# Performance work log

Hardware: AMD Instinct MI355X
Metric: run time of the kernel (lower is better)

## Reference

```python
import jax, jax.numpy as jnp
import numpy as np

EPS = 1e-5


def setup_inputs() -> dict:
    key = jax.random.key(0)
    ks = jax.random.split(key, 12)
    B, C, H, W = 1, 512, 64, 64
    d = C // 8
    inp = {
        "x": jax.random.normal(ks[0], (B, C, H, W), jnp.float32),
        "y": jax.random.normal(ks[1], (B, C, H, W), jnp.float32),
        "s_m": jax.random.uniform(ks[2], (H, W), jnp.float32),
        "q_m": jax.random.uniform(ks[3], (H, W), jnp.float32),
        "Wq": jax.random.normal(ks[4], (d, C), jnp.float32) * (1.0 / np.sqrt(C)),
        "bq": jnp.zeros((d,), jnp.float32),
        "Wk": jax.random.normal(ks[5], (d, C), jnp.float32) * (1.0 / np.sqrt(C)),
        "bk": jnp.zeros((d,), jnp.float32),
        "Wv": jax.random.normal(ks[6], (C, C), jnp.float32) * (1.0 / np.sqrt(C)),
        "bv": jnp.zeros((C,), jnp.float32),
        "W1": jax.random.normal(ks[7], (C, C), jnp.float32) * (1.0 / np.sqrt(C)),
        "b1": jnp.zeros((C,), jnp.float32),
        "W2": jax.random.normal(ks[8], (C, C), jnp.float32) * (1.0 / np.sqrt(C)),
        "b2": jnp.zeros((C,), jnp.float32),
        "gamma": jnp.ones((1, C, H, W), jnp.float32),
        "beta": jnp.zeros((1, C, H, W), jnp.float32),
    }
    return inp


def _conv1x1(x, Wt, b):
    # 1x1 Conv2d == per-pixel channel matmul
    return jnp.einsum("bchw,oc->bohw", x, Wt) + b[None, :, None, None]


def reference(x, y, s_m, q_m, Wq, bq, Wk, bk, Wv, bv, W1, b1, W2, b2, gamma, beta):
    B, C, H, W = x.shape
    N = H * W
    scale = (C // 8) ** (-0.5)

    q_m = jnp.where(q_m > 0.8, 1.0, 0.0).astype(x.dtype)
    x_fg = x * s_m[None, None]
    y_fg = y * q_m[None, None]

    def branch(q_in, k_in, v_in, use_max):
        q = _conv1x1(q_in, Wq, bq).reshape(B, -1, N).transpose(0, 2, 1) * scale  # [B,N,d]
        k = _conv1x1(k_in, Wk, bk).reshape(B, -1, N)                             # [B,d,N]
        v = _conv1x1(v_in, Wv, bv).reshape(B, -1, N)                             # [B,C,N]
        attn = jnp.einsum("bqd,bdk->bqk", q, k)                                  # [B,N,N]
        stat = jnp.max(attn) if use_max else jnp.min(attn)
        thr = (stat + jnp.mean(attn)) * 0.5
        attn = jnp.where(attn < thr, jnp.asarray(-999.0, attn.dtype), attn)
        attn = jax.nn.softmax(attn, axis=-1)
        out = jnp.einsum("bck,bqk->bcq", v, attn).reshape(B, C, H, W)
        h = out.transpose(0, 2, 3, 1)                                            # [B,H,W,C]
        h = jnp.maximum(h @ W1.T + b1, 0.0) @ W2.T + b2
        out = h.transpose(0, 3, 1, 2)
        # LayerNorm over all trailing dims [1,C,H,W] (B==1)
        mu = jnp.mean(out)
        var = jnp.mean((out - mu) ** 2)
        out = (out - mu) * jax.lax.rsqrt(var + EPS) * gamma + beta
        return out

    outx = branch(x_fg, y_fg, y_fg, True)
    outx = outx * s_m[None, None] + x * (1.0 - s_m)[None, None]
    outy = branch(y_fg, x, x, False)
    outy = outy * q_m[None, None] + y * (1.0 - q_m)[None, None]
    return outx, outy
```

## Files before the change

### kernel.cpp

```cpp
#include <hip/hip_runtime.h>
#include <math.h>

#define C_DIM 512
#define N_DIM 4096
#define CN (C_DIM * N_DIM)
#define SZO (N_DIM * C_DIM)
#define NN ((size_t)N_DIM * N_DIM)
#define NN_TOT ((long long)N_DIM * N_DIM)

typedef __attribute__((ext_vector_type(4))) float f32x4;
typedef __attribute__((ext_vector_type(8))) short short8;

__device__ __forceinline__ ushort f2bf(float f) {
    unsigned u = __float_as_uint(f);
    unsigned r = u + 0x7FFFu + ((u >> 16) & 1u);
    return (ushort)(r >> 16);
}
__device__ __forceinline__ float bf2f(ushort h) {
    return __uint_as_float((unsigned)h << 16);
}

__device__ __forceinline__ void gload16(const void* g, void* l) {
    __builtin_amdgcn_global_load_lds(
        (const __attribute__((address_space(1))) void*)g,
        (__attribute__((address_space(3))) void*)l, 16, 0, 0);
}

__global__ __launch_bounds__(256) void setup_all(
    const float* __restrict__ x, const float* __restrict__ y,
    ushort* __restrict__ xbT, ushort* __restrict__ ybT,
    const float* __restrict__ Wv, const float* __restrict__ W1,
    const float* __restrict__ W2, ushort* __restrict__ Wvb,
    ushort* __restrict__ W1b, ushort* __restrict__ W2b,
    const float* __restrict__ Wq, const float* __restrict__ Wk,
    float* __restrict__ PX)
{
    __shared__ float t[64][65];
    __shared__ float Asw[16][130];
    __shared__ float Bsx[16][65];
    const int id = blockIdx.x;
    const int tid = threadIdx.x;

    if (id < 1024) {
        const int bx = id & 63, by = (id >> 6) & 7, bz = id >> 9;
        const float* X = bz ? y : x;
        ushort* XT = bz ? ybT : xbT;
        const int c0 = bx * 64, r0 = by * 64;
        const int ty = tid >> 4, tx = tid & 15;
        #pragma unroll
        for (int i = 0; i < 4; ++i) {
            int r = ty + i * 16;
            float4 v = *(const float4*)&X[(size_t)(r0 + r) * N_DIM + c0 + tx * 4];
            t[r][tx * 4 + 0] = v.x; t[r][tx * 4 + 1] = v.y;
            t[r][tx * 4 + 2] = v.z; t[r][tx * 4 + 3] = v.w;
        }
        __syncthreads();
        #pragma unroll
        for (int i = 0; i < 4; ++i) {
            int nn = ty + i * 16;
            ushort4 o;
            o.x = f2bf(t[tx * 4 + 0][nn]); o.y = f2bf(t[tx * 4 + 1][nn]);
            o.z = f2bf(t[tx * 4 + 2][nn]); o.w = f2bf(t[tx * 4 + 3][nn]);
            *(ushort4*)&XT[(size_t)(c0 + nn) * C_DIM + r0 + tx * 4] = o;
        }
        return;
    }
    if (id < 1792) {
        const int i2 = id - 1024;
        const int bx = i2 & 255, by = i2 >> 8;
        const float* in  = (by == 0) ? Wv : (by == 1) ? W1 : W2;
        ushort*      out = (by == 0) ? Wvb : (by == 1) ? W1b : W2b;
        int i = (bx * 256 + tid) * 4;
        float4 v = *(const float4*)&in[i];
        ushort4 o = { f2bf(v.x), f2bf(v.y), f2bf(v.z), f2bf(v.w) };
        *(ushort4*)&out[i] = o;
        return;
    }
    {
        const int i3 = id - 1792;
        const int ntile = i3 & 63;
        const int srcT  = (i3 >> 6) & 1;
        const int kz    = i3 >> 7;
        const float* X = srcT ? y : x;
        const int n0 = ntile * 64;
        const int ty = tid >> 4, tx = tid & 15;
        float accQ[4][4] = {}, accK[4][4] = {};
        const int kbase = kz * 256;

        for (int k0 = kbase; k0 < kbase + 256; k0 += 16) {
            #pragma unroll
            for (int i = 0; i < 2; ++i) {
                int wi = tid + i * 256;
                int mm = wi >> 2;
                int kq = (wi & 3) * 4;
                const float* Wp = (mm < 64) ? &Wq[(size_t)mm * 512]
                                            : &Wk[(size_t)(mm - 64) * 512];
                float4 w4 = *(const float4*)&Wp[k0 + kq];
                Asw[kq + 0][mm] = w4.x; Asw[kq + 1][mm] = w4.y;
                Asw[kq + 2][mm] = w4.z; Asw[kq + 3][mm] = w4.w;
            }
            {
                int kk = tid >> 4, nq = (tid & 15) * 4;
                *(float4*)&Bsx[kk][nq] = *(const float4*)&X[(size_t)(k0 + kk) * N_DIM + n0 + nq];
            }
            __syncthreads();
            #pragma unroll
            for (int kk = 0; kk < 16; ++kk) {
                float aq[4], ak[4], b[4];
                #pragma unroll
                for (int r = 0; r < 4; ++r) { aq[r] = Asw[kk][ty * 4 + r]; ak[r] = Asw[kk][64 + ty * 4 + r]; }
                #pragma unroll
                for (int c = 0; c < 4; ++c) b[c] = Bsx[kk][tx * 4 + c];
                #pragma unroll
                for (int r = 0; r < 4; ++r)
                    #pragma unroll
                    for (int c = 0; c < 4; ++c) {
                        accQ[r][c] = fmaf(aq[r], b[c], accQ[r][c]);
                        accK[r][c] = fmaf(ak[r], b[c], accK[r][c]);
                    }
            }
            __syncthreads();
        }
        float* dst = PX + ((size_t)(kz * 2 + srcT) * 128) * N_DIM;
        #pragma unroll
        for (int r = 0; r < 4; ++r) {
            float4 oq = make_float4(accQ[r][0], accQ[r][1], accQ[r][2], accQ[r][3]);
            *(float4*)&dst[(size_t)(ty * 4 + r) * N_DIM + n0 + tx * 4] = oq;
            float4 ok = make_float4(accK[r][0], accK[r][1], accK[r][2], accK[r][3]);
            *(float4*)&dst[(size_t)(64 + ty * 4 + r) * N_DIM + n0 + tx * 4] = ok;
        }
    }
}

__global__ __launch_bounds__(256) void qkfinish(
    const float* __restrict__ PX,
    const float* __restrict__ s_m, const float* __restrict__ q_m,
    const float* __restrict__ bq, const float* __restrict__ bk,
    ushort* __restrict__ QF0, ushort* __restrict__ KF0,
    ushort* __restrict__ QF1, ushort* __restrict__ KF1)
{
    int gid = blockIdx.x * 256 + threadIdx.x;
    int lane = gid & 63;
    int rest = gid >> 6;
    int blk = rest & 255;
    int tensor = rest >> 8;
    int fr = lane & 15, quad = lane >> 4;
    int n = blk * 16 + fr;

    int srcT, rowbase, isQ;
    const float* bias;
    ushort* dst;
    float mv, scale;
    if (tensor == 0)      { srcT = 0; rowbase = 0;  isQ = 1; bias = bq; dst = QF0; scale = 0.125f; mv = s_m[n]; }
    else if (tensor == 1) { srcT = 1; rowbase = 64; isQ = 0; bias = bk; dst = KF0; scale = 1.0f;   mv = (q_m[n] > 0.8f) ? 1.0f : 0.0f; }
    else if (tensor == 2) { srcT = 1; rowbase = 0;  isQ = 1; bias = bq; dst = QF1; scale = 0.125f; mv = (q_m[n] > 0.8f) ? 1.0f : 0.0f; }
    else                  { srcT = 0; rowbase = 64; isQ = 0; bias = bk; dst = KF1; scale = 1.0f;   mv = 1.0f; }

    ushort hi0[8], lo0[8], hi1[8], lo1[8];
    #pragma unroll
    for (int j = 0; j < 8; ++j) {
        int d0 = quad * 8 + j, d1 = 32 + d0;
        float v0 = 0.0f, v1 = 0.0f;
        #pragma unroll
        for (int kz = 0; kz < 2; ++kz) {
            size_t base = ((size_t)(kz * 2 + srcT) * 128 + rowbase);
            v0 += PX[(base + d0) * N_DIM + n];
            v1 += PX[(base + d1) * N_DIM + n];
        }
        v0 = (v0 * mv + bias[d0]) * scale;
        v1 = (v1 * mv + bias[d1]) * scale;
        hi0[j] = f2bf(v0); lo0[j] = f2bf(v0 - bf2f(hi0[j]));
        hi1[j] = f2bf(v1); lo1[j] = f2bf(v1 - bf2f(hi1[j]));
    }
    auto wr8 = [&](int kstep, const ushort* v) {
        size_t base = ((size_t)(blk * 6 + kstep) * 64 + lane) * 8;
        *(ushort4*)&dst[base]     = *(const ushort4*)&v[0];
        *(ushort4*)&dst[base + 4] = *(const ushort4*)&v[4];
    };
    wr8(0, hi0); wr8(1, hi1);
    if (isQ) { wr8(2, hi0); wr8(3, hi1); wr8(4, lo0); wr8(5, lo1); }
    else     { wr8(2, lo0); wr8(3, lo1); wr8(4, hi0); wr8(5, hi1); }
}

__device__ __forceinline__ void scores_mfma(
    const ushort* __restrict__ QF, const ushort* __restrict__ KF,
    int m0, int n0, int wr, int wc, int lane, f32x4 acc[4][4])
{
    const int blkA0 = (m0 + wr) >> 4;
    const int blkB0 = (n0 + wc) >> 4;
    #pragma unroll
    for (int s = 0; s < 6; ++s) {
        short8 af[4], bf[4];
        #pragma unroll
        for (int mr = 0; mr < 4; ++mr)
            af[mr] = *(const short8*)&QF[((size_t)((blkA0 + mr) * 6 + s) * 64 + lane) * 8];
        #pragma unroll
        for (int nc = 0; nc < 4; ++nc)
            bf[nc] = *(const short8*)&KF[((size_t)((blkB0 + nc) * 6 + s) * 64 + lane) * 8];
        #pragma unroll
        for (int mr = 0; mr < 4; ++mr)
            #pragma unroll
            for (int nc = 0; nc < 4; ++nc)
                acc[mr][nc] = __builtin_amdgcn_mfma_f32_16x16x32_bf16(
                    af[mr], bf[nc], acc[mr][nc], 0, 0, 0);
    }
}

__global__ __launch_bounds__(256) void vproj_p1(
    const ushort* __restrict__ Wvb,
    const ushort* __restrict__ xbT, const ushort* __restrict__ ybT,
    const float* __restrict__ bv, const float* __restrict__ q_m,
    ushort* __restrict__ Vb,
    const ushort* __restrict__ QF0, const ushort* __restrict__ KF0,
    const ushort* __restrict__ QF1, const ushort* __restrict__ KF1,
    float* __restrict__ part, float* __restrict__ rowmaxp)
{
    __shared__ ushort As[2][128 * 32];
    __shared__ ushort Bs[2][128 * 32];
    __shared__ float wrm[2][128];
    __shared__ float red[256];
    const int id = blockIdx.x;
    const int tid = threadIdx.x;
    const int lane = tid & 63;
    const int wid  = tid >> 6;

    if (id < 256) {
        const int bxn = id & 31;
        const int bym = (id >> 5) & 3;
        const int br  = id >> 7;
        const ushort* A = Wvb;
        const ushort* B = br ? xbT : ybT;
        const int m0 = bym * 128, n0 = bxn * 128;
        const int wr = (wid >> 1) * 64, wc = (wid & 1) * 64;
        const int lrow = lane >> 2;
        const int kbl  = lane & 3;
        const int K = 512;

        auto stage = [&](int buf, int t) {
            #pragma unroll
            for (int c = wid; c < 16; c += 4) {
                if (c < 8) {
                    int r = c * 16 + lrow;
                    int kb = kbl ^ ((r >> 1) & 3);
                    gload16(A + (size_t)(m0 + r) * K + t * 32 + kb * 8, &As[buf][c * 512]);
                } else {
                    int cb = c - 8;
                    int r = cb * 16 + lrow;
                    int kb = kbl ^ ((r >> 1) & 3);
                    gload16(B + (size_t)(n0 + r) * K + t * 32 + kb * 8, &Bs[buf][cb * 512]);
                }
            }
        };

        f32x4 acc[4][4] = {};
        const int fr = lane & 15;
        const int kq = lane >> 4;
        stage(0, 0);
        asm volatile("s_waitcnt vmcnt(0)" ::: "memory");
        __syncthreads();
        int cur = 0;
        for (int t = 0; t < 16; ++t) {
            if (t + 1 < 16) stage(cur ^ 1, t + 1);
            short8 af[4], bf[4];
            #pragma unroll
            for (int mr = 0; mr < 4; ++mr) {
                int rA = wr + mr * 16 + fr;
                af[mr] = *(const short8*)&As[cur][rA * 32 + (kq ^ ((rA >> 1) & 3)) * 8];
            }
            #pragma unroll
            for (int nc = 0; nc < 4; ++nc) {
                int rB = wc + nc * 16 + fr;
                bf[nc] = *(const short8*)&Bs[cur][rB * 32 + (kq ^ ((rB >> 1) & 3)) * 8];
            }
            #pragma unroll
            for (int mr = 0; mr < 4; ++mr)
                #pragma unroll
                for (int nc = 0; nc < 4; ++nc)
                    acc[mr][nc] = __builtin_amdgcn_mfma_f32_16x16x32_bf16(
                        af[mr], bf[nc], acc[mr][nc], 0, 0, 0);
            asm volatile("s_waitcnt vmcnt(0)" ::: "memory");
            __syncthreads();
            cur ^= 1;
        }
        const int orow = (lane >> 4) * 4;
        const int ocol = lane & 15;
        float mcol[4];
        #pragma unroll
        for (int nc = 0; nc < 4; ++nc) {
            int gn = n0 + wc + nc * 16 + ocol;
            mcol[nc] = br ? 1.0f : ((q_m[gn] > 0.8f) ? 1.0f : 0.0f);
        }
        ushort* Obf = Vb + (size_t)br * CN;
        #pragma unroll
        for (int mr = 0; mr < 4; ++mr)
            #pragma unroll
            for (int j = 0; j < 4; ++j) {
                int gm = m0 + wr + mr * 16 + orow + j;
                float brow = bv[gm];
                #pragma unroll
                for (int nc = 0; nc < 4; ++nc) {
                    int gn = n0 + wc + nc * 16 + ocol;
                    float v = acc[mr][nc][j] * mcol[nc] + brow;
                    Obf[(size_t)gm * N_DIM + gn] = f2bf(v);
                }
            }
        return;
    }

    {
        const int p = id - 256;
        const int bxn = p & 31;
        const int bym = (p >> 5) & 31;
        const int br  = p >> 10;
        const ushort* QF = br ? QF1 : QF0;
        const ushort* KF = br ? KF1 : KF0;
        float* pt = part + (size_t)br * 3072;
        float* rmp = rowmaxp + (size_t)br * 131072;

        const int m0 = bym * 128, n0 = bxn * 128;
        const int wr = (wid >> 1) * 64, wc = (wid & 1) * 64;
        f32x4 acc[4][4] = {};
        scores_mfma(QF, KF, m0, n0, wr, wc, lane, acc);

        float lmax = -3.4e38f, lmin = 3.4e38f, lsum = 0.0f;
        float rmx[4][4];
        #pragma unroll
        for (int mr = 0; mr < 4; ++mr)
            #pragma unroll
            for (int j = 0; j < 4; ++j) rmx[mr][j] = -3.4e38f;
        #pragma unroll
        for (int mr = 0; mr < 4; ++mr)
            #pragma unroll
            for (int nc = 0; nc < 4; ++nc)
                #pragma unroll
                for (int j = 0; j < 4; ++j) {
                    float v = acc[mr][nc][j];
                    lsum += v; lmax = fmaxf(lmax, v); lmin = fminf(lmin, v);
                    rmx[mr][j] = fmaxf(rmx[mr][j], v);
                }
        #pragma unroll
        for (int m = 1; m < 16; m <<= 1)
            #pragma unroll
            for (int mr = 0; mr < 4; ++mr)
                #pragma unroll
                for (int j = 0; j < 4; ++j)
                    rmx[mr][j] = fmaxf(rmx[mr][j], __shfl_xor(rmx[mr][j], m, 64));

        const int orow = (lane >> 4) * 4;
        if ((lane & 15) == 0) {
            #pragma unroll
            for (int mr = 0; mr < 4; ++mr)
                #pragma unroll
                for (int j = 0; j < 4; ++j)
                    wrm[wid & 1][wr + mr * 16 + orow + j] = rmx[mr][j];
        }
        __syncthreads();
        if (tid < 128) {
            float v = fmaxf(wrm[0][tid], wrm[1][tid]);
            rmp[(size_t)bxn * 4096 + m0 + tid] = v;
        }

        const int bid = bym * 32 + bxn;
        __syncthreads();
        red[tid] = lmax; __syncthreads();
        for (int s = 128; s > 0; s >>= 1) { if (tid < s) red[tid] = fmaxf(red[tid], red[tid + s]); __syncthreads(); }
        if (tid == 0) pt[bid] = red[0];
        __syncthreads();
        red[tid] = lmin; __syncthreads();
        for (int s = 128; s > 0; s >>= 1) { if (tid < s) red[tid] = fminf(red[tid], red[tid + s]); __syncthreads(); }
        if (tid == 0) pt[1024 + bid] = red[0];
        __syncthreads();
        red[tid] = lsum; __syncthreads();
        for (int s = 128; s > 0; s >>= 1) { if (tid < s) red[tid] += red[tid + s]; __syncthreads(); }
        if (tid == 0) pt[2048 + bid] = red[0];
    }
}

__global__ __launch_bounds__(256) void stats_fin2(
    const float* __restrict__ part, float* __restrict__ stats)
{
    const int br = blockIdx.x;
    part += (size_t)br * 3072;
    __shared__ float rmax[256], rmin[256];
    __shared__ double rsum[256];
    int tid = threadIdx.x;
    float m1 = -3.4e38f, m2 = 3.4e38f; double s = 0.0;
    for (int i = tid; i < 1024; i += 256) {
        m1 = fmaxf(m1, part[i]);
        m2 = fminf(m2, part[1024 + i]);
        s += (double)part[2048 + i];
    }
    rmax[tid] = m1; rmin[tid] = m2; rsum[tid] = s;
    __syncthreads();
    for (int st = 128; st > 0; st >>= 1) {
        if (tid < st) {
            rmax[tid] = fmaxf(rmax[tid], rmax[tid + st]);
            rmin[tid] = fminf(rmin[tid], rmin[tid + st]);
            rsum[tid] += rsum[tid + st];
        }
        __syncthreads();
    }
    if (tid == 0) {
        float stat = (br == 0) ? rmax[0] : rmin[0];
        float mean = (float)(rsum[0] / (double)NN_TOT);
        stats[br] = 0.5f * (stat + mean);
    }
}

__global__ __launch_bounds__(256) void scores_pass2(
    const ushort* __restrict__ QF0, const ushort* __restrict__ KF0,
    const ushort* __restrict__ QF1, const ushort* __restrict__ KF1,
    const float* __restrict__ stats, const float* __restrict__ rowmaxp,
    ushort* __restrict__ Pe, float* __restrict__ rowsump)
{
    const int br = blockIdx.z;
    const ushort* QF = br ? QF1 : QF0;
    const ushort* KF = br ? KF1 : KF0;
    ushort* P = Pe + (size_t)br * NN;
    rowsump += (size_t)br * 131072;
    rowmaxp += (size_t)br * 131072;

    const int tid = threadIdx.x;
    const int lane = tid & 63, wid = tid >> 6;
    const int m0 = blockIdx.y * 128, n0 = blockIdx.x * 128;
    const int wr = (wid >> 1) * 64, wc = (wid & 1) * 64;
    const float thr = stats[br];

    __shared__ float rowmL[128];
    if (tid < 128) {
        int r = m0 + tid;
        float m = -3.4e38f;
        #pragma unroll 8
        for (int b = 0; b < 32; ++b)
            m = fmaxf(m, rowmaxp[(size_t)b * 4096 + r]);
        rowmL[tid] = (m >= thr) ? m : -1e30f;
    }
    __syncthreads();

    f32x4 acc[4][4] = {};
    scores_mfma(QF, KF, m0, n0, wr, wc, lane, acc);

    const int orow = (lane >> 4) * 4;
    const int ocol = lane & 15;
    float rm[4][4], rs[4][4];
    #pragma unroll
    for (int mr = 0; mr < 4; ++mr)
        #pragma unroll
        for (int j = 0; j < 4; ++j) {
            rm[mr][j] = rowmL[wr + mr * 16 + orow + j];
            rs[mr][j] = 0.0f;
        }
    #pragma unroll
    for (int mr = 0; mr < 4; ++mr)
        #pragma unroll
        for (int nc = 0; nc < 4; ++nc)
            #pragma unroll
            for (int j = 0; j < 4; ++j) {
                float s = acc[mr][nc][j];
                float m = rm[mr][j];
                float e = (s < thr) ? 0.0f : __expf(s - m);
                if (m < -1e29f) e = 1.0f;
                ushort h = f2bf(e);
                rs[mr][j] += bf2f(h);
                P[(size_t)(m0 + wr + mr * 16 + orow + j) * N_DIM
                  + n0 + wc + nc * 16 + ocol] = h;
            }
    #pragma unroll
    for (int m = 1; m < 16; m <<= 1)
        #pragma unroll
        for (int mr = 0; mr < 4; ++mr)
            #pragma unroll
            for (int j = 0; j < 4; ++j)
                rs[mr][j] += __shfl_xor(rs[mr][j], m, 64);

    __shared__ float wrs[2][128];
    if ((lane & 15) == 0) {
        #pragma unroll
        for (int mr = 0; mr < 4; ++mr)
            #pragma unroll
            for (int j = 0; j < 4; ++j)
                wrs[wid & 1][wr + mr * 16 + orow + j] = rs[mr][j];
    }
    __syncthreads();
    if (tid < 128)
        rowsump[(size_t)blockIdx.x * 4096 + m0 + tid] =
            wrs[0][tid] + wrs[1][tid];
}

template<int BM, int BN>
__global__ __launch_bounds__(256) void mfma_g(
    const ushort* __restrict__ A0, const ushort* __restrict__ A1,
    const ushort* __restrict__ B0, const ushort* __restrict__ B1,
    void* __restrict__ Out, size_t outBrStride,
    int M, int N, int K, int kLen, int nkz, int swapxy,
    const float* __restrict__ bias, int biasMode,
    const float* __restrict__ mask0, int mm0,
    const float* __restrict__ mask1, int mm1,
    int doRelu, int outBf16, float* __restrict__ lnp)
{
    constexpr int WAVES_M = BM / 64;
    constexpr int WAVES_N = 4 / WAVES_M;
    constexpr int WN = BN / WAVES_N;
    constexpr int FM = 4;
    constexpr int FN = WN / 16;
    constexpr int NCHUNK = (BM + BN) / 16;

    __shared__ ushort As[2][BM * 32];
    __shared__ ushort Bs[2][BN * 32];
    const int tid  = threadIdx.x;
    const int lane = tid & 63;
    const int wid  = tid >> 6;
    const int z  = blockIdx.z;
    const int br = z / nkz;
    const int kz = z % nkz;
    const ushort* A = br ? A1 : A0;
    const ushort* B = br ? B1 : B0;
    const float* mask = br ? mask1 : mask0;
    const int maskMode = br ? mm1 : mm0;

    const int bxm = swapxy ? blockIdx.x : blockIdx.y;
    const int bxn = swapxy ? blockIdx.y : blockIdx.x;
    const int m0 = bxm * BM, n0 = bxn * BN;
    const int wm = wid / WAVES_N, wn = wid % WAVES_N;
    const int wr = wm * 64, wc = wn * WN;
    const int kOff = kz * kLen;
    const int lrow = lane >> 2;
    const int kbl  = lane & 3;

    auto stage = [&](int buf, int t) {
        #pragma unroll
        for (int c = wid; c < NCHUNK; c += 4) {
            if (c < BM / 16) {
                int r = c * 16 + lrow;
                int kb = kbl ^ ((r >> 1) & 3);
                gload16(A + (size_t)(m0 + r) * K + kOff + t * 32 + kb * 8,
                        &As[buf][c * 512]);
            } else {
                int cb = c - BM / 16;
                int r = cb * 16 + lrow;
                int kb = kbl ^ ((r >> 1) & 3);
                gload16(B + (size_t)(n0 + r) * K + kOff + t * 32 + kb * 8,
                        &Bs[buf][cb * 512]);
            }
        }
    };

    f32x4 acc[FM][FN] = {};
    const int fr = lane & 15;
    const int kq = lane >> 4;
    const int nt = kLen / 32;

    stage(0, 0);
    asm volatile("s_waitcnt vmcnt(0)" ::: "memory");
    __syncthreads();
    int cur = 0;
    for (int t = 0; t < nt; ++t) {
        if (t + 1 < nt) stage(cur ^ 1, t + 1);
        short8 af[FM], bf[FN];
        #pragma unroll
        for (int mr = 0; mr < FM; ++mr) {
            int rA = wr + mr * 16 + fr;
            af[mr] = *(const short8*)&As[cur][rA * 32 + (kq ^ ((rA >> 1) & 3)) * 8];
        }
        #pragma unroll
        for (int nc = 0; nc < FN; ++nc) {
            int rB = wc + nc * 16 + fr;
            bf[nc] = *(const short8*)&Bs[cur][rB * 32 + (kq ^ ((rB >> 1) & 3)) * 8];
        }
        #pragma unroll
        for (int mr = 0; mr < FM; ++mr)
            #pragma unroll
            for (int nc = 0; nc < FN; ++nc)
                acc[mr][nc] = __builtin_amdgcn_mfma_f32_16x16x32_bf16(
                    af[mr], bf[nc], acc[mr][nc], 0, 0, 0);
        asm volatile("s_waitcnt vmcnt(0)" ::: "memory");
        __syncthreads();
        cur ^= 1;
    }

    const int orow = (lane >> 4) * 4;
    const int ocol = lane & 15;

    if (nkz > 1) {
        float* Of = (float*)Out + (size_t)z * M * N;
        #pragma unroll
        for (int mr = 0; mr < FM; ++mr)
            #pragma unroll
            for (int nc = 0; nc < FN; ++nc)
                #pragma unroll
                for (int j = 0; j < 4; ++j) {
                    int gm = m0 + wr + mr * 16 + orow + j;
                    int gn = n0 + wc + nc * 16 + ocol;
                    Of[(size_t)gm * N + gn] = acc[mr][nc][j];
                }
        return;
    }

    float mcol[FN], bcol[FN];
    #pragma unroll
    for (int nc = 0; nc < FN; ++nc) {
        int gn = n0 + wc + nc * 16 + ocol;
        mcol[nc] = (maskMode == 0) ? 1.0f
                 : (maskMode == 1) ? mask[gn]
                                   : (mask[gn] > 0.8f ? 1.0f : 0.0f);
        bcol[nc] = (biasMode == 2) ? bias[gn] : 0.0f;
    }
    ushort* Obf = (ushort*)Out + (size_t)br * outBrStride;
    float*  Of  = (float*)Out + (size_t)br * outBrStride;
    float lsum = 0.0f, lsq = 0.0f;
    #pragma unroll
    for (int mr = 0; mr < FM; ++mr) {
        #pragma unroll
        for (int j = 0; j < 4; ++j) {
            int gm = m0 + wr + mr * 16 + orow + j;
            float brow = (biasMode == 1) ? bias[gm] : 0.0f;
            #pragma unroll
            for (int nc = 0; nc < FN; ++nc) {
                int gn = n0 + wc + nc * 16 + ocol;
                float v = acc[mr][nc][j] * mcol[nc] + brow + bcol[nc];
                if (doRelu) v = fmaxf(v, 0.0f);
                if (outBf16) Obf[(size_t)gm * N + gn] = f2bf(v);
                else         Of[(size_t)gm * N + gn] = v;
                lsum += v; lsq = fmaf(v, v, lsq);
            }
        }
    }
    if (lnp) {
        __shared__ float redS[256], redQ[256];
        redS[tid] = lsum; redQ[tid] = lsq;
        __syncthreads();
        for (int s = 128; s > 0; s >>= 1) {
            if (tid < s) { redS[tid] += redS[tid + s]; redQ[tid] += redQ[tid + s]; }
            __syncthreads();
        }
        if (tid == 0) {
            int fb = blockIdx.y * gridDim.x + blockIdx.x;
            lnp[br * 512 + fb] = redS[0];
            lnp[br * 512 + 256 + fb] = redQ[0];
        }
    }
}

__global__ __launch_bounds__(256) void reduce2row(
    const float* __restrict__ P4, const float* __restrict__ rowsump,
    ushort* __restrict__ O)
{
    const int br = blockIdx.y;
    const int tid = threadIdx.x;
    const int r0 = blockIdx.x * 2;
    __shared__ float invL[2];
    if (tid < 64) {
        int rw = tid >> 5, b = tid & 31;
        float s = rowsump[(size_t)br * 131072 + (size_t)b * 4096 + r0 + rw];
        #pragma unroll
        for (int m = 1; m < 32; m <<= 1) s += __shfl_xor(s, m, 64);
        if (b == 0) invL[rw] = 1.0f / s;
    }
    __syncthreads();
    int i = (blockIdx.x * 256 + tid) * 4;
    float sc = invL[(i >> 9) & 1];
    float4 a = *(const float4*)&P4[(size_t)(br * 2 + 0) * SZO + i];
    float4 b = *(const float4*)&P4[(size_t)(br * 2 + 1) * SZO + i];
    ushort4 o;
    o.x = f2bf((a.x + b.x) * sc);
    o.y = f2bf((a.y + b.y) * sc);
    o.z = f2bf((a.z + b.z) * sc);
    o.w = f2bf((a.w + b.w) * sc);
    *(ushort4*)&O[(size_t)br * SZO + i] = o;
}

__global__ __launch_bounds__(256) void gate_write(
    const float* __restrict__ H2, const float* __restrict__ lnp,
    const float* __restrict__ gamma, const float* __restrict__ beta,
    const float* __restrict__ x, const float* __restrict__ y,
    const float* __restrict__ s_m, const float* __restrict__ q_m,
    float* __restrict__ out)
{
    const int br = blockIdx.y;
    const int tid = threadIdx.x;
    __shared__ double rs[256], rq[256];
    rs[tid] = (double)lnp[(size_t)br * 512 + tid];
    rq[tid] = (double)lnp[(size_t)br * 512 + 256 + tid];
    __syncthreads();
    for (int st = 128; st > 0; st >>= 1) {
        if (tid < st) { rs[tid] += rs[tid + st]; rq[tid] += rq[tid + st]; }
        __syncthreads();
    }
    double muD = rs[0] / (double)CN;
    double varD = rq[0] / (double)CN - muD * muD;
    float mu = (float)muD;
    float rstd = (float)(1.0 / sqrt(varD + 1e-5));

    size_t i = ((size_t)blockIdx.x * 256 + tid) * 4;
    int n = (int)(i & (N_DIM - 1));
    float4 h = *(const float4*)&H2[(size_t)br * CN + i];
    float4 g = *(const float4*)&gamma[i];
    float4 b = *(const float4*)&beta[i];
    const float* resid = br ? y : x;
    float4 r = *(const float4*)&resid[i];
    float vals[4] = { h.x, h.y, h.z, h.w };
    float gs[4] = { g.x, g.y, g.z, g.w };
    float bs[4] = { b.x, b.y, b.z, b.w };
    float rsv[4] = { r.x, r.y, r.z, r.w };
    float os[4];
    #pragma unroll
    for (int j = 0; j < 4; ++j) {
        float mv = br ? ((q_m[n + j] > 0.8f) ? 1.0f : 0.0f) : s_m[n + j];
        float normed = (vals[j] - mu) * rstd * gs[j] + bs[j];
        os[j] = normed * mv + rsv[j] * (1.0f - mv);
    }
    float4 o; o.x = os[0]; o.y = os[1]; o.z = os[2]; o.w = os[3];
    *(float4*)&out[(size_t)br * CN + i] = o;
}

extern "C" void kernel_launch(void* const* d_in, const int* in_sizes, int n_in,
                              void* d_out, int out_size, void* d_ws, size_t ws_size,
                              hipStream_t stream)
{
    const float* x     = (const float*)d_in[0];
    const float* y     = (const float*)d_in[1];
    const float* s_m   = (const float*)d_in[2];
    const float* q_m   = (const float*)d_in[3];
    const float* Wq    = (const float*)d_in[4];
    const float* bq    = (const float*)d_in[5];
    const float* Wk    = (const float*)d_in[6];
    const float* bk    = (const float*)d_in[7];
    const float* Wv    = (const float*)d_in[8];
    const float* bv    = (const float*)d_in[9];
    const float* W1    = (const float*)d_in[10];
    const float* b1    = (const float*)d_in[11];
    const float* W2    = (const float*)d_in[12];
    const float* b2    = (const float*)d_in[13];
    const float* gamma = (const float*)d_in[14];
    const float* beta  = (const float*)d_in[15];
    float* out = (float*)d_out;

    float* ws = (float*)d_ws;
    float*  R1    = ws;
    float*  PX    = R1;
    float*  P4    = R1;
    ushort* QF0   = (ushort*)(R1 + 4194304);
    ushort* KF0   = QF0 + 786432;
    ushort* QF1   = KF0 + 786432;
    ushort* KF1   = QF1 + 786432;
    float*  SMALL = R1 + 8388608;
    float*  PART  = SMALL;
    float*  RMAXP = PART + 6144;
    float*  RSUMP = RMAXP + 262144;
    float*  LNP   = RSUMP + 262144;
    float*  STATS = LNP + 1024;
    ushort* Wvb   = (ushort*)(STATS + 64);
    ushort* W1b   = Wvb + 262144;
    ushort* W2b   = W1b + 262144;
    ushort* Vb    = W2b + 262144;
    ushort* R2    = Vb + 4194304;
    ushort* xbT   = R2;
    ushort* ybT   = R2 + 2097152;
    ushort* Pe    = R2;
    ushort* O1T   = R2;
    ushort* H1T   = R2 + 4194304;
    float*  H2    = (float*)(R2 + 8388608);

    setup_all<<<2048, 256, 0, stream>>>(
        x, y, xbT, ybT, Wv, W1, W2, Wvb, W1b, W2b, Wq, Wk, PX);

    qkfinish<<<256, 256, 0, stream>>>(PX, s_m, q_m, bq, bk, QF0, KF0, QF1, KF1);

    vproj_p1<<<2304, 256, 0, stream>>>(
        Wvb, xbT, ybT, bv, q_m, Vb, QF0, KF0, QF1, KF1, PART, RMAXP);

    stats_fin2<<<2, 256, 0, stream>>>(PART, STATS);

    scores_pass2<<<dim3(32, 32, 2), 256, 0, stream>>>(
        QF0, KF0, QF1, KF1, STATS, RMAXP, Pe, RSUMP);

    mfma_g<128, 128><<<dim3(32, 4, 4), 256, 0, stream>>>(
        Pe, Pe + NN, Vb, Vb + CN, P4, 0,
        4096, 512, 4096, 2048, 2, 1, nullptr, 0, nullptr, 0, nullptr, 0, 0, 0, nullptr);

    reduce2row<<<dim3(2048, 2), 256, 0, stream>>>(P4, RSUMP, O1T);

    mfma_g<128, 64><<<dim3(32, 8, 2), 256, 0, stream>>>(
        O1T, O1T + SZO, W1b, W1b, H1T, (size_t)SZO,
        4096, 512, 512, 512, 1, 1, b1, 2, nullptr, 0, nullptr, 0, 1, 1, nullptr);

    mfma_g<64, 128><<<dim3(32, 8, 2), 256, 0, stream>>>(
        W2b, W2b, H1T, H1T + SZO, H2, (size_t)CN,
        512, 4096, 512, 512, 1, 0, b2, 1, nullptr, 0, nullptr, 0, 0, 0, LNP);

    gate_write<<<dim3(2048, 2), 256, 0, stream>>>(
        H2, LNP, gamma, beta, x, y, s_m, q_m, out);
}
```

Before: 258.4 us.

## Move Q/K projection to split-bf16 MFMA GEMM kernel

```diff
diff --git a/kernel.cpp b/kernel.cpp
--- a/kernel.cpp
+++ b/kernel.cpp
@@ -26,25 +26,25 @@
         (__attribute__((address_space(3))) void*)l, 16, 0, 0);
 }
 
-__global__ __launch_bounds__(256) void setup_all(
+__global__ __launch_bounds__(256) void setup2(
     const float* __restrict__ x, const float* __restrict__ y,
-    ushort* __restrict__ xbT, ushort* __restrict__ ybT,
+    ushort* __restrict__ xbT, ushort* __restrict__ xlT,
+    ushort* __restrict__ ybT, ushort* __restrict__ ylT,
     const float* __restrict__ Wv, const float* __restrict__ W1,
     const float* __restrict__ W2, ushort* __restrict__ Wvb,
     ushort* __restrict__ W1b, ushort* __restrict__ W2b,
     const float* __restrict__ Wq, const float* __restrict__ Wk,
-    float* __restrict__ PX)
+    ushort* __restrict__ WqkH, ushort* __restrict__ WqkL)
 {
     __shared__ float t[64][65];
-    __shared__ float Asw[16][130];
-    __shared__ float Bsx[16][65];
     const int id = blockIdx.x;
     const int tid = threadIdx.x;
 
     if (id < 1024) {
         const int bx = id & 63, by = (id >> 6) & 7, bz = id >> 9;
         const float* X = bz ? y : x;
-        ushort* XT = bz ? ybT : xbT;
+        ushort* XH = bz ? ybT : xbT;
+        ushort* XL = bz ? ylT : xlT;
         const int c0 = bx * 64, r0 = by * 64;
         const int ty = tid >> 4, tx = tid & 15;
         #pragma unroll
@@ -58,10 +58,15 @@
         #pragma unroll
         for (int i = 0; i < 4; ++i) {
             int nn = ty + i * 16;
-            ushort4 o;
-            o.x = f2bf(t[tx * 4 + 0][nn]); o.y = f2bf(t[tx * 4 + 1][nn]);
-            o.z = f2bf(t[tx * 4 + 2][nn]); o.w = f2bf(t[tx * 4 + 3][nn]);
-            *(ushort4*)&XT[(size_t)(c0 + nn) * C_DIM + r0 + tx * 4] = o;
+            ushort4 h, l;
+            float v0 = t[tx * 4 + 0][nn], v1 = t[tx * 4 + 1][nn];
+            float v2 = t[tx * 4 + 2][nn], v3 = t[tx * 4 + 3][nn];
+            h.x = f2bf(v0); h.y = f2bf(v1); h.z = f2bf(v2); h.w = f2bf(v3);
+            l.x = f2bf(v0 - bf2f(h.x)); l.y = f2bf(v1 - bf2f(h.y));
+            l.z = f2bf(v2 - bf2f(h.z)); l.w = f2bf(v3 - bf2f(h.w));
+            size_t off = (size_t)(c0 + nn) * C_DIM + r0 + tx * 4;
+            *(ushort4*)&XH[off] = h;
+            *(ushort4*)&XL[off] = l;
         }
         return;
     }
@@ -77,59 +82,106 @@
         return;
     }
     {
-        const int i3 = id - 1792;
-        const int ntile = i3 & 63;
-        const int srcT  = (i3 >> 6) & 1;
-        const int kz    = i3 >> 7;
-        const float* X = srcT ? y : x;
-        const int n0 = ntile * 64;
-        const int ty = tid >> 4, tx = tid & 15;
-        float accQ[4][4] = {}, accK[4][4] = {};
-        const int kbase = kz * 256;
-
-        for (int k0 = kbase; k0 < kbase + 256; k0 += 16) {
-            #pragma unroll
-            for (int i = 0; i < 2; ++i) {
-                int wi = tid + i * 256;
-                int mm = wi >> 2;
-                int kq = (wi & 3) * 4;
-                const float* Wp = (mm < 64) ? &Wq[(size_t)mm * 512]
-                                            : &Wk[(size_t)(mm - 64) * 512];
-                float4 w4 = *(const float4*)&Wp[k0 + kq];
-                Asw[kq + 0][mm] = w4.x; Asw[kq + 1][mm] = w4.y;
-                Asw[kq + 2][mm] = w4.z; Asw[kq + 3][mm] = w4.w;
+        const int bx = id - 1792;
+        int i = (bx * 256 + tid) * 4;
+        int row = i >> 9;
+        const float* src = (row < 64) ? &Wq[(size_t)row * 512]
+                                      : &Wk[(size_t)(row - 64) * 512];
+        float4 v = *(const float4*)&src[i & 511];
+        ushort4 h, l;
+        h.x = f2bf(v.x); h.y = f2bf(v.y); h.z = f2bf(v.z); h.w = f2bf(v.w);
+        l.x = f2bf(v.x - bf2f(h.x)); l.y = f2bf(v.y - bf2f(h.y));
+        l.z = f2bf(v.z - bf2f(h.z)); l.w = f2bf(v.w - bf2f(h.w));
+        *(ushort4*)&WqkH[i] = h;
+        *(ushort4*)&WqkL[i] = l;
+    }
+}
+
+__global__ __launch_bounds__(256) void qkproj(
+    const ushort* __restrict__ WqkH, const ushort* __restrict__ WqkL,
+    const ushort* __restrict__ xbT, const ushort* __restrict__ xlT,
+    const ushort* __restrict__ ybT, const ushort* __restrict__ ylT,
+    float* __restrict__ PX)
+{
+    __shared__ ushort As[2][128 * 32];
+    __shared__ ushort Bs[2][128 * 32];
+    const int tid = threadIdx.x;
+    const int lane = tid & 63;
+    const int wid  = tid >> 6;
+    const int n0  = blockIdx.x * 128;
+    const int kz  = blockIdx.y;
+    const int src = blockIdx.z;
+    const ushort* XH = src ? ybT : xbT;
+    const ushort* XL = src ? ylT : xlT;
+    const int wr = (wid >> 1) * 64, wc = (wid & 1) * 64;
+    const int lrow = lane >> 2;
+    const int kbl  = lane & 3;
+
+    auto stage = [&](int buf, int tt) {
+        const ushort* Asrc = (tt >= 32) ? WqkL : WqkH;
+        const ushort* Bsrc = (tt >= 16 && tt < 32) ? XL : XH;
+        const int ko = (tt & 15) * 32;
+        #pragma unroll
+        for (int c = wid; c < 16; c += 4) {
+            if (c < 8) {
+                int r = c * 16 + lrow;
+                int kb = kbl ^ ((r >> 1) & 3);
+                gload16(Asrc + (size_t)r * 512 + ko + kb * 8, &As[buf][c * 512]);
+            } else {
+                int cb = c - 8;
+                int r = cb * 16 + lrow;
+                int kb = kbl ^ ((r >> 1) & 3);
+                gload16(Bsrc + (size_t)(n0 + r) * 512 + ko + kb * 8, &Bs[buf][cb * 512]);
             }
-            {
-                int kk = tid >> 4, nq = (tid & 15) * 4;
-                *(float4*)&Bsx[kk][nq] = *(const float4*)&X[(size_t)(k0 + kk) * N_DIM + n0 + nq];
+        }
+    };
+
+    f32x4 acc[4][4] = {};
+    const int fr = lane & 15;
+    const int kq = lane >> 4;
+    const int t0 = kz * 12;
+
+    stage(0, t0);
+    asm volatile("s_waitcnt vmcnt(0)" ::: "memory");
+    __syncthreads();
+    int cur = 0;
+    for (int s = 0; s < 12; ++s) {
+        if (s + 1 < 12) stage(cur ^ 1, t0 + s + 1);
+        short8 af[4], bf[4];
+        #pragma unroll
+        for (int mr = 0; mr < 4; ++mr) {
+            int rA = wr + mr * 16 + fr;
+            af[mr] = *(const short8*)&As[cur][rA * 32 + (kq ^ ((rA >> 1) & 3)) * 8];
+        }
+        #pragma unroll
+        for (int nc = 0; nc < 4; ++nc) {
+            int rB = wc + nc * 16 + fr;
+            bf[nc] = *(const short8*)&Bs[cur][rB * 32 + (kq ^ ((rB >> 1) & 3)) * 8];
+        }
+        #pragma unroll
+        for (int mr = 0; mr < 4; ++mr)
+            #pragma unroll
+            for (int nc = 0; nc < 4; ++nc)
+                acc[mr][nc] = __builtin_amdgcn_mfma_f32_16x16x32_bf16(
+                    af[mr], bf[nc], acc[mr][nc], 0, 0, 0);
+        asm volatile("s_waitcnt vmcnt(0)" ::: "memory");
+        __syncthreads();
+        cur ^= 1;
+    }
+
+    const int orow = (lane >> 4) * 4;
+    const int ocol = lane & 15;
+    float* Of = PX + ((size_t)(kz * 2 + src) * 128) * N_DIM;
+    #pragma unroll
+    for (int mr = 0; mr < 4; ++mr)
+        #pragma unroll
+        for (int nc = 0; nc < 4; ++nc)
+            #pragma unroll
+            for (int j = 0; j < 4; ++j) {
+                int gm = wr + mr * 16 + orow + j;
+                int gn = n0 + wc + nc * 16 + ocol;
+                Of[(size_t)gm * N_DIM + gn] = acc[mr][nc][j];
             }
-            __syncthreads();
-            #pragma unroll
-            for (int kk = 0; kk < 16; ++kk) {
-                float aq[4], ak[4], b[4];
-                #pragma unroll
-                for (int r = 0; r < 4; ++r) { aq[r] = Asw[kk][ty * 4 + r]; ak[r] = Asw[kk][64 + ty * 4 + r]; }
-                #pragma unroll
-                for (int c = 0; c < 4; ++c) b[c] = Bsx[kk][tx * 4 + c];
-                #pragma unroll
-                for (int r = 0; r < 4; ++r)
-                    #pragma unroll
-                    for (int c = 0; c < 4; ++c) {
-                        accQ[r][c] = fmaf(aq[r], b[c], accQ[r][c]);
-                        accK[r][c] = fmaf(ak[r], b[c], accK[r][c]);
-                    }
-            }
-            __syncthreads();
-        }
-        float* dst = PX + ((size_t)(kz * 2 + srcT) * 128) * N_DIM;
-        #pragma unroll
-        for (int r = 0; r < 4; ++r) {
-            float4 oq = make_float4(accQ[r][0], accQ[r][1], accQ[r][2], accQ[r][3]);
-            *(float4*)&dst[(size_t)(ty * 4 + r) * N_DIM + n0 + tx * 4] = oq;
-            float4 ok = make_float4(accK[r][0], accK[r][1], accK[r][2], accK[r][3]);
-            *(float4*)&dst[(size_t)(64 + ty * 4 + r) * N_DIM + n0 + tx * 4] = ok;
-        }
-    }
 }
 
 __global__ __launch_bounds__(256) void qkfinish(
@@ -162,7 +214,7 @@
         int d0 = quad * 8 + j, d1 = 32 + d0;
         float v0 = 0.0f, v1 = 0.0f;
         #pragma unroll
-        for (int kz = 0; kz < 2; ++kz) {
+        for (int kz = 0; kz < 4; ++kz) {
             size_t base = ((size_t)(kz * 2 + srcT) * 128 + rowbase);
             v0 += PX[(base + d0) * N_DIM + n];
             v1 += PX[(base + d1) * N_DIM + n];
@@ -749,20 +801,28 @@
     float*  RSUMP = RMAXP + 262144;
     float*  LNP   = RSUMP + 262144;
     float*  STATS = LNP + 1024;
-    ushort* Wvb   = (ushort*)(STATS + 64);
+    ushort* WqkH  = (ushort*)(STATS + 64);
+    ushort* WqkL  = WqkH + 65536;
+    ushort* Wvb   = WqkL + 65536;
     ushort* W1b   = Wvb + 262144;
     ushort* W2b   = W1b + 262144;
     ushort* Vb    = W2b + 262144;
     ushort* R2    = Vb + 4194304;
     ushort* xbT   = R2;
     ushort* ybT   = R2 + 2097152;
+    ushort* xlT   = R2 + 4194304;
+    ushort* ylT   = R2 + 6291456;
     ushort* Pe    = R2;
     ushort* O1T   = R2;
     ushort* H1T   = R2 + 4194304;
     float*  H2    = (float*)(R2 + 8388608);
 
-    setup_all<<<2048, 256, 0, stream>>>(
-        x, y, xbT, ybT, Wv, W1, W2, Wvb, W1b, W2b, Wq, Wk, PX);
+    setup2<<<1856, 256, 0, stream>>>(
+        x, y, xbT, xlT, ybT, ylT, Wv, W1, W2, Wvb, W1b, W2b,
+        Wq, Wk, WqkH, WqkL);
+
+    qkproj<<<dim3(32, 4, 2), 256, 0, stream>>>(
+        WqkH, WqkL, xbT, xlT, ybT, ylT, PX);
 
     qkfinish<<<256, 256, 0, stream>>>(PX, s_m, q_m, bq, bk, QF0, KF0, QF1, KF1);
 
```

Result: faster. 230.2 us (median of 2 runs) (-10.9%).
